# Performance work log

Measured on AMD Instinct MI355X. Metric: run time of the kernel, lower is better.

Reference implementation:

```python
import jax, jax.numpy as jnp
import numpy as np

D_MODEL = 1024
D_FF = 4096
N_EXPERTS = 8
TOP_K = 2
AUX_COEF = 0.01
ZLOSS_COEF = 0.001
EPS = 1e-9


def setup_inputs() -> dict:
    key = jax.random.key(0)
    k0, k1, k2, k3 = jax.random.split(key, 4)
    x = jax.random.normal(k0, (4, 2048, D_MODEL), dtype=jnp.float32)
    router_w = jax.random.normal(k1, (N_EXPERTS, D_MODEL), dtype=jnp.float32) * 0.02
    w1 = jax.random.normal(k2, (N_EXPERTS, D_FF, D_MODEL), dtype=jnp.float32) * 0.02
    b1 = jnp.zeros((N_EXPERTS, D_FF), dtype=jnp.float32)
    w2 = jax.random.normal(k3, (N_EXPERTS, D_MODEL, D_FF), dtype=jnp.float32) * 0.02
    b2 = jnp.zeros((N_EXPERTS, D_MODEL), dtype=jnp.float32)
    return {"x": x, "router_w": router_w, "w1": w1, "b1": b1, "w2": w2, "b2": b2}


def reference(x, router_w, w1, b1, w2, b2):
    B, T, D = x.shape
    N = B * T
    xf = x.reshape(N, D)

    # Router: logits [N, E], softmax probs, top-k selection + renormalized weights
    logits = jnp.einsum('nd,ed->ne', xf, router_w)
    probs = jax.nn.softmax(logits, axis=-1)
    topk_vals, topk_idx = jax.lax.top_k(probs, TOP_K)  # [N, K]
    topk_w = topk_vals / (topk_vals.sum(axis=-1, keepdims=True) + EPS)

    # Dense combine weights [N, E] (top-k indices are unique per row)
    combine = jnp.zeros((N, N_EXPERTS), dtype=xf.dtype)
    combine = combine.at[jnp.arange(N)[:, None], topk_idx].add(topk_w)

    # Per-expert MLP (fixed small loop over experts), weighted combine.
    # drop_tokens=False => no capacity truncation; masked-dense == gather/scatter math.
    y = jnp.zeros_like(xf)
    for e in range(N_EXPERTS):
        h = jax.nn.gelu(jnp.einsum('nd,fd->nf', xf, w1[e]) + b1[e], approximate=False)
        out_e = jnp.einsum('nf,df->nd', h, w2[e]) + b2[e]
        y = y + out_e * combine[:, e:e + 1]

    # Aux losses / stats
    importance = probs.sum(axis=0)                                   # [E]
    expert_load = jnp.zeros((N_EXPERTS,), jnp.float32).at[topk_idx.reshape(-1)].add(1.0)
    imp_n = importance / (importance.sum() + EPS)
    load_n = expert_load / (expert_load.sum() + EPS)
    balance_loss = N_EXPERTS * jnp.sum(imp_n * load_n)
    z_loss = jnp.mean(jax.nn.logsumexp(logits, axis=-1) ** 2)
    aux_loss = AUX_COEF * balance_loss + ZLOSS_COEF * z_loss

    return y.reshape(B, T, D), aux_loss, expert_load, importance
```

## Files before the change

### kernel.cpp

```cpp
#include <hip/hip_runtime.h>
#include <math.h>

#define NTOK 8192
#define DMODEL 1024
#define DFF 4096
#define NEXP 8
#define TILE 128
#define MAXTILES 136
#define MAXROWS (MAXTILES * TILE)
#define MOE_EPS 1e-9f
#define REG 4096

typedef unsigned short u16;
typedef __bf16 bf16x8 __attribute__((ext_vector_type(8)));
typedef float f32x4 __attribute__((ext_vector_type(4)));

struct Ctrl {
    int counts[NEXP];
    int fill[NEXP];
    int padded_off[NEXP];
    int n_tiles;
    int tile_expert[MAXTILES];
    int tile_base[MAXTILES];
    int tile_valid[MAXTILES];
    float imp[NEXP];
    float zacc;
};

__device__ __forceinline__ u16 f2bf(float f) {
    unsigned u = __float_as_uint(f);
    unsigned r = u + 0x7fffu + ((u >> 16) & 1u);
    return (u16)(r >> 16);
}

__device__ __forceinline__ void load16(const void* g, void* l) {
    __builtin_amdgcn_global_load_lds((__attribute__((address_space(1))) void*)g,
                                     (__attribute__((address_space(3))) void*)l,
                                     16, 0, 0);
}

__device__ __forceinline__ float gelu_fast(float h) {
    float u = h * (1.5957691216f + 0.0713548162f * h * h);
    return h / (1.f + __expf(-u));
}

__global__ __launch_bounds__(256) void k_convert(const float* __restrict__ src,
                                                 u16* __restrict__ dst, int n4) {
    int i = blockIdx.x * 256 + threadIdx.x;
    int stride = gridDim.x * 256;
    for (; i < n4; i += stride) {
        float4 v = ((const float4*)src)[i];
        ushort4 o;
        o.x = f2bf(v.x); o.y = f2bf(v.y); o.z = f2bf(v.z); o.w = f2bf(v.w);
        ((ushort4*)dst)[i] = o;
    }
}

__global__ __launch_bounds__(256) void k_router(const float* __restrict__ x,
                                                const float* __restrict__ rw,
                                                u16* __restrict__ xb,
                                                int* __restrict__ top_idx,
                                                float* __restrict__ top_w,
                                                Ctrl* __restrict__ ctrl) {
    __shared__ float srw[NEXP * DMODEL];
    __shared__ float simp[NEXP];
    __shared__ float szl;
    int tid = threadIdx.x;
    for (int i = tid; i < NEXP * DMODEL / 4; i += 256)
        ((float4*)srw)[i] = ((const float4*)rw)[i];
    if (tid < NEXP) simp[tid] = 0.f;
    if (tid == 0) szl = 0.f;
    __syncthreads();

    int lane = tid & 63;
    int n = blockIdx.x * 4 + (tid >> 6);
    float p[NEXP];
#pragma unroll
    for (int e = 0; e < NEXP; ++e) p[e] = 0.f;
    const float4* xr = (const float4*)(x + (size_t)n * DMODEL);
    u16 xs[16];
#pragma unroll
    for (int j = 0; j < 4; ++j) {
        float4 xv = xr[lane * 4 + j];
        int d = (lane * 4 + j) * 4;
        xs[j * 4 + 0] = f2bf(xv.x);
        xs[j * 4 + 1] = f2bf(xv.y);
        xs[j * 4 + 2] = f2bf(xv.z);
        xs[j * 4 + 3] = f2bf(xv.w);
#pragma unroll
        for (int e = 0; e < NEXP; ++e) {
            const float* r = srw + e * DMODEL + d;
            p[e] += xv.x * r[0] + xv.y * r[1] + xv.z * r[2] + xv.w * r[3];
        }
    }
    {
        uint4* dst = (uint4*)(xb + (size_t)n * DMODEL + lane * 16);
        dst[0] = ((const uint4*)xs)[0];
        dst[1] = ((const uint4*)xs)[1];
    }
#pragma unroll
    for (int e = 0; e < NEXP; ++e) {
#pragma unroll
        for (int off = 32; off > 0; off >>= 1) p[e] += __shfl_xor(p[e], off);
    }
    if (lane == 0) {
        float m = p[0];
#pragma unroll
        for (int e = 1; e < NEXP; ++e) m = fmaxf(m, p[e]);
        float pr[NEXP];
        float s = 0.f;
#pragma unroll
        for (int e = 0; e < NEXP; ++e) { pr[e] = expf(p[e] - m); s += pr[e]; }
        float inv = 1.f / s;
#pragma unroll
        for (int e = 0; e < NEXP; ++e) pr[e] *= inv;
        float lse = m + logf(s);
        int i0 = 0; float v0 = pr[0];
#pragma unroll
        for (int e = 1; e < NEXP; ++e) if (pr[e] > v0) { v0 = pr[e]; i0 = e; }
        int i1 = -1; float v1 = -1.f;
#pragma unroll
        for (int e = 0; e < NEXP; ++e) if (e != i0 && pr[e] > v1) { v1 = pr[e]; i1 = e; }
        float den = v0 + v1 + MOE_EPS;
        top_idx[n * 2] = i0;
        top_idx[n * 2 + 1] = i1;
        top_w[n * 2] = v0 / den;
        top_w[n * 2 + 1] = v1 / den;
#pragma unroll
        for (int e = 0; e < NEXP; ++e) atomicAdd(&simp[e], pr[e]);
        atomicAdd(&szl, lse * lse);
    }
    __syncthreads();
    if (tid < NEXP) atomicAdd(&ctrl->imp[tid], simp[tid]);
    if (tid == 255) atomicAdd(&ctrl->zacc, szl);
}

__global__ __launch_bounds__(256) void k_build(const int* __restrict__ top_idx,
                                               Ctrl* __restrict__ ctrl,
                                               int* __restrict__ tok_idx,
                                               float* __restrict__ tok_w) {
    __shared__ int cnt[NEXP];
    __shared__ int off[NEXP];
    __shared__ int tiles[NEXP];
    int tid = threadIdx.x;
    if (tid < NEXP) cnt[tid] = 0;
    __syncthreads();
    for (int i = tid; i < NTOK * 2; i += 256) atomicAdd(&cnt[top_idx[i]], 1);
    __syncthreads();
    if (tid == 0) {
        int o = 0, t = 0;
        for (int e = 0; e < NEXP; ++e) {
            int c = cnt[e];
            int te = (c + TILE - 1) / TILE;
            ctrl->counts[e] = c;
            ctrl->padded_off[e] = o;
            off[e] = o;
            tiles[e] = te;
            for (int i = 0; i < te; ++i) {
                ctrl->tile_expert[t] = e;
                ctrl->tile_base[t] = o + i * TILE;
                int v = c - i * TILE;
                ctrl->tile_valid[t] = v > TILE ? TILE : v;
                ++t;
            }
            o += te * TILE;
        }
        ctrl->n_tiles = t;
    }
    __syncthreads();
    for (int e = 0; e < NEXP; ++e) {
        int start = off[e] + cnt[e];
        int end = off[e] + tiles[e] * TILE;
        for (int i = start + tid; i < end; i += 256) {
            tok_idx[i] = 0;
            tok_w[i] = 0.f;
        }
    }
}

__global__ __launch_bounds__(256) void k_fill(const int* __restrict__ top_idx,
                                              const float* __restrict__ top_w,
                                              Ctrl* __restrict__ ctrl,
                                              int* __restrict__ tok_idx,
                                              float* __restrict__ tok_w) {
    int n = blockIdx.x * 256 + threadIdx.x;
    if (n >= NTOK) return;
#pragma unroll
    for (int k = 0; k < 2; ++k) {
        int e = top_idx[n * 2 + k];
        int pos = atomicAdd(&ctrl->fill[e], 1);
        int slot = ctrl->padded_off[e] + pos;
        tok_idx[slot] = n;
        tok_w[slot] = top_w[n * 2 + k];
    }
}

#define KLOOP3(STA, STB, NK)                                                          \
    STA(0, 0); STB(0, 0);                                                             \
    STA(1, 1); STB(1, 1);                                                             \
    for (int kt = 0; kt < (NK); ++kt) {                                               \
        int p = kt & 1;                                                               \
        if (kt < (NK) - 1) asm volatile("s_waitcnt vmcnt(4)" ::: "memory");           \
        else               asm volatile("s_waitcnt vmcnt(0)" ::: "memory");           \
        __builtin_amdgcn_s_barrier();                                                 \
        const u16* Ar = sA + p * REG;                                                 \
        const u16* Br = sB + p * REG;                                                 \
        bf16x8 a[4], b[4];                                                            \
        _Pragma("unroll") for (int m = 0; m < 4; ++m) a[m] = *(const bf16x8*)(Ar + aoff[m]); \
        _Pragma("unroll") for (int n = 0; n < 4; ++n) b[n] = *(const bf16x8*)(Br + boff[n]); \
        __builtin_amdgcn_s_setprio(1);                                                \
        _Pragma("unroll") for (int m = 0; m < 4; ++m)                                 \
            _Pragma("unroll") for (int n = 0; n < 4; ++n)                             \
                acc[m][n] = __builtin_amdgcn_mfma_f32_16x16x32_bf16(a[m], b[n], acc[m][n], 0, 0, 0); \
        __builtin_amdgcn_s_setprio(0);                                                \
        __builtin_amdgcn_s_barrier();                                                 \
        if (kt + 2 < (NK)) { STA(p, kt + 2); STB(p, kt + 2); }                        \
    }

__global__ __launch_bounds__(256, 4) void k_gemm1(const u16* __restrict__ xb,
                                                  const u16* __restrict__ w1b,
                                                  const float* __restrict__ b1,
                                                  const int* __restrict__ tok_idx,
                                                  const Ctrl* __restrict__ ctrl,
                                                  u16* __restrict__ H) {
    int flat = blockIdx.x;
    int t = (flat & 7) + ((flat >> 8) << 3);
    int n0 = ((flat >> 3) & 31) * TILE;
    if (t >= ctrl->n_tiles) return;
    int e = ctrl->tile_expert[t];
    int rbase = ctrl->tile_base[t];

    __shared__ __align__(16) u16 sA[2 * REG];
    __shared__ __align__(16) u16 sB[2 * REG];

    int tid = threadIdx.x;
    const u16* aS[2];
    const u16* bS[2];
    int fo[2];
#pragma unroll
    for (int q = 0; q < 2; ++q) {
        int f = q * 256 + tid;
        int row = f >> 2;
        int lc = (f & 3) ^ ((row >> 1) & 3);
        aS[q] = xb + (size_t)tok_idx[rbase + row] * DMODEL + lc * 8;
        bS[q] = w1b + (size_t)e * DFF * DMODEL + (size_t)(n0 + row) * DMODEL + lc * 8;
        fo[q] = f * 8;
    }

#define STA1(pp, kt)                                                                  \
    do { _Pragma("unroll") for (int q = 0; q < 2; ++q)                                \
        load16(aS[q] + (kt) * 32, &sA[(pp) * REG + fo[q]]); } while (0)
#define STB1(pp, kt)                                                                  \
    do { _Pragma("unroll") for (int q = 0; q < 2; ++q)                                \
        load16(bS[q] + (kt) * 32, &sB[(pp) * REG + fo[q]]); } while (0)

    int lane = tid & 63, w = tid >> 6;
    int wr = w >> 1, wc = w & 1;
    int l15 = lane & 15, lg = lane >> 4;
    int csw = (lg ^ ((l15 >> 1) & 3)) * 8;

    int aoff[4], boff[4];
#pragma unroll
    for (int m = 0; m < 4; ++m) aoff[m] = (wr * 64 + m * 16 + l15) * 32 + csw;
#pragma unroll
    for (int n = 0; n < 4; ++n) boff[n] = (wc * 64 + n * 16 + l15) * 32 + csw;

    f32x4 acc[4][4];
#pragma unroll
    for (int m = 0; m < 4; ++m)
#pragma unroll
        for (int n = 0; n < 4; ++n) acc[m][n] = (f32x4){0.f, 0.f, 0.f, 0.f};

    KLOOP3(STA1, STB1, DMODEL / 32)
#undef STA1
#undef STB1

    float bias[4];
#pragma unroll
    for (int n = 0; n < 4; ++n) bias[n] = b1[e * DFF + n0 + wc * 64 + n * 16 + l15];
#pragma unroll
    for (int m = 0; m < 4; ++m)
#pragma unroll
        for (int n = 0; n < 4; ++n) {
            int gcol = n0 + wc * 64 + n * 16 + l15;
#pragma unroll
            for (int r = 0; r < 4; ++r) {
                int grow = wr * 64 + m * 16 + lg * 4 + r;
                float h = acc[m][n][r] + bias[n];
                H[(size_t)(rbase + grow) * DFF + gcol] = f2bf(gelu_fast(h));
            }
        }
}

__global__ __launch_bounds__(256, 4) void k_gemm2(const u16* __restrict__ H,
                                                  const u16* __restrict__ w2b,
                                                  const float* __restrict__ b2,
                                                  const int* __restrict__ tok_idx,
                                                  const float* __restrict__ tok_w,
                                                  const Ctrl* __restrict__ ctrl,
                                                  float* __restrict__ y) {
    int flat = blockIdx.x;
    int t = (flat & 7) + ((flat >> 6) << 3);
    int n0 = ((flat >> 3) & 7) * TILE;
    if (t >= ctrl->n_tiles) return;
    int e = ctrl->tile_expert[t];
    int rbase = ctrl->tile_base[t];
    int valid = ctrl->tile_valid[t];

    __shared__ __align__(16) u16 sA[2 * REG];
    __shared__ __align__(16) u16 sB[2 * REG];

    int tid = threadIdx.x;
    const u16* aS[2];
    const u16* bS[2];
    int fo[2];
#pragma unroll
    for (int q = 0; q < 2; ++q) {
        int f = q * 256 + tid;
        int row = f >> 2;
        int lc = (f & 3) ^ ((row >> 1) & 3);
        aS[q] = H + (size_t)(rbase + row) * DFF + lc * 8;
        bS[q] = w2b + (size_t)e * DMODEL * DFF + (size_t)(n0 + row) * DFF + lc * 8;
        fo[q] = f * 8;
    }

#define STA2(pp, kt)                                                                  \
    do { _Pragma("unroll") for (int q = 0; q < 2; ++q)                                \
        load16(aS[q] + (kt) * 32, &sA[(pp) * REG + fo[q]]); } while (0)
#define STB2(pp, kt)                                                                  \
    do { _Pragma("unroll") for (int q = 0; q < 2; ++q)                                \
        load16(bS[q] + (kt) * 32, &sB[(pp) * REG + fo[q]]); } while (0)

    int lane = tid & 63, w = tid >> 6;
    int wr = w >> 1, wc = w & 1;
    int l15 = lane & 15, lg = lane >> 4;
    int csw = (lg ^ ((l15 >> 1) & 3)) * 8;

    int aoff[4], boff[4];
#pragma unroll
    for (int m = 0; m < 4; ++m) aoff[m] = (wr * 64 + m * 16 + l15) * 32 + csw;
#pragma unroll
    for (int n = 0; n < 4; ++n) boff[n] = (wc * 64 + n * 16 + l15) * 32 + csw;

    f32x4 acc[4][4];
#pragma unroll
    for (int m = 0; m < 4; ++m)
#pragma unroll
        for (int n = 0; n < 4; ++n) acc[m][n] = (f32x4){0.f, 0.f, 0.f, 0.f};

    KLOOP3(STA2, STB2, DFF / 32)
#undef STA2
#undef STB2

    float bias[4];
#pragma unroll
    for (int n = 0; n < 4; ++n) bias[n] = b2[e * DMODEL + n0 + wc * 64 + n * 16 + l15];
#pragma unroll
    for (int m = 0; m < 4; ++m)
#pragma unroll
        for (int n = 0; n < 4; ++n) {
            int gcol = n0 + wc * 64 + n * 16 + l15;
#pragma unroll
            for (int r = 0; r < 4; ++r) {
                int grow = wr * 64 + m * 16 + lg * 4 + r;
                if (grow < valid) {
                    int slot = rbase + grow;
                    int tok = tok_idx[slot];
                    float wgt = tok_w[slot];
                    unsafeAtomicAdd(&y[(size_t)tok * DMODEL + gcol],
                                    wgt * (acc[m][n][r] + bias[n]));
                }
            }
        }
}

__global__ void k_final(const Ctrl* __restrict__ ctrl, float* __restrict__ out) {
    if (blockIdx.x == 0 && threadIdx.x == 0) {
        float imp[NEXP], ld[NEXP];
        float imps = 0.f, loads = 0.f;
        for (int e = 0; e < NEXP; ++e) {
            imp[e] = ctrl->imp[e];
            ld[e] = (float)ctrl->counts[e];
            imps += imp[e];
            loads += ld[e];
        }
        float bal = 0.f;
        for (int e = 0; e < NEXP; ++e)
            bal += (imp[e] / (imps + MOE_EPS)) * (ld[e] / (loads + MOE_EPS));
        bal *= (float)NEXP;
        float z = ctrl->zacc / (float)NTOK;
        float aux = 0.01f * bal + 0.001f * z;
        size_t base = (size_t)NTOK * DMODEL;
        out[base] = aux;
        for (int e = 0; e < NEXP; ++e) out[base + 1 + e] = ld[e];
        for (int e = 0; e < NEXP; ++e) out[base + 9 + e] = imp[e];
    }
}

extern "C" void kernel_launch(void* const* d_in, const int* in_sizes, int n_in,
                              void* d_out, int out_size, void* d_ws, size_t ws_size,
                              hipStream_t stream) {
    (void)in_sizes; (void)n_in; (void)out_size; (void)ws_size;
    const float* x  = (const float*)d_in[0];
    const float* rw = (const float*)d_in[1];
    const float* w1 = (const float*)d_in[2];
    const float* b1 = (const float*)d_in[3];
    const float* w2 = (const float*)d_in[4];
    const float* b2 = (const float*)d_in[5];
    float* out = (float*)d_out;

    char* p = (char*)d_ws;
    Ctrl* ctrl = (Ctrl*)p;          p += 4096;
    u16* xb    = (u16*)p;           p += (size_t)NTOK * DMODEL * 2;
    u16* w1b   = (u16*)p;           p += (size_t)NEXP * DFF * DMODEL * 2;
    u16* w2b   = (u16*)p;           p += (size_t)NEXP * DMODEL * DFF * 2;
    u16* Hbuf  = (u16*)p;           p += (size_t)MAXROWS * DFF * 2;
    int* tok_idx = (int*)p;         p += (size_t)MAXROWS * 4;
    float* tok_w = (float*)p;       p += (size_t)MAXROWS * 4;
    int* tIdx  = (int*)p;           p += (size_t)NTOK * 2 * 4;
    float* tW  = (float*)p;         p += (size_t)NTOK * 2 * 4;

    hipMemsetAsync(ctrl, 0, sizeof(Ctrl), stream);
    hipMemsetAsync(d_out, 0, (size_t)NTOK * DMODEL * sizeof(float), stream);

    k_convert<<<2048, 256, 0, stream>>>(w1, w1b, NEXP * DFF * DMODEL / 4);
    k_convert<<<2048, 256, 0, stream>>>(w2, w2b, NEXP * DMODEL * DFF / 4);

    k_router<<<NTOK / 4, 256, 0, stream>>>(x, rw, xb, tIdx, tW, ctrl);
    k_build<<<1, 256, 0, stream>>>(tIdx, ctrl, tok_idx, tok_w);
    k_fill<<<NTOK / 256, 256, 0, stream>>>(tIdx, tW, ctrl, tok_idx, tok_w);

    k_gemm1<<<MAXTILES * (DFF / TILE), 256, 0, stream>>>(xb, w1b, b1, tok_idx, ctrl, Hbuf);
    k_gemm2<<<MAXTILES * (DMODEL / TILE), 256, 0, stream>>>(Hbuf, w2b, b2, tok_idx, tok_w, ctrl, out);

    k_final<<<1, 64, 0, stream>>>(ctrl, out);
}
```

Before: 750.5 us.

## Widen GEMM tiles to 128x256 with 512-thread blocks and 8 waves

Both expert GEMM kernels move from 128x128 output tiles with 4 waves to 128x256 tiles with 8 waves (a 2x4 wave grid). Each block now loads one A chunk per thread and a doubled B tile, so each A row fetched from shared memory is reused across twice as many output columns and the grid shrinks by half. The change raises shared memory per block to 48KB and puts 512 threads in a block, which may lower the number of resident blocks per CU and increase per-barrier synchronisation cost.

```diff
diff --git a/kernel.cpp b/kernel.cpp
--- a/kernel.cpp
+++ b/kernel.cpp
@@ -6,10 +6,12 @@
 #define DFF 4096
 #define NEXP 8
 #define TILE 128
+#define BN 256
 #define MAXTILES 136
 #define MAXROWS (MAXTILES * TILE)
 #define MOE_EPS 1e-9f
-#define REG 4096
+#define REGA 4096
+#define REGB 8192
 
 typedef unsigned short u16;
 typedef __bf16 bf16x8 __attribute__((ext_vector_type(8)));
@@ -195,16 +197,16 @@
     }
 }
 
-#define KLOOP3(STA, STB, NK)                                                          \
+#define KLOOP4(STA, STB, NK)                                                          \
     STA(0, 0); STB(0, 0);                                                             \
     STA(1, 1); STB(1, 1);                                                             \
     for (int kt = 0; kt < (NK); ++kt) {                                               \
         int p = kt & 1;                                                               \
-        if (kt < (NK) - 1) asm volatile("s_waitcnt vmcnt(4)" ::: "memory");           \
+        if (kt < (NK) - 1) asm volatile("s_waitcnt vmcnt(3)" ::: "memory");           \
         else               asm volatile("s_waitcnt vmcnt(0)" ::: "memory");           \
         __builtin_amdgcn_s_barrier();                                                 \
-        const u16* Ar = sA + p * REG;                                                 \
-        const u16* Br = sB + p * REG;                                                 \
+        const u16* Ar = sA + p * REGA;                                                \
+        const u16* Br = sB + p * REGB;                                                \
         bf16x8 a[4], b[4];                                                            \
         _Pragma("unroll") for (int m = 0; m < 4; ++m) a[m] = *(const bf16x8*)(Ar + aoff[m]); \
         _Pragma("unroll") for (int n = 0; n < 4; ++n) b[n] = *(const bf16x8*)(Br + boff[n]); \
@@ -217,45 +219,49 @@
         if (kt + 2 < (NK)) { STA(p, kt + 2); STB(p, kt + 2); }                        \
     }
 
-__global__ __launch_bounds__(256, 4) void k_gemm1(const u16* __restrict__ xb,
+__global__ __launch_bounds__(512, 4) void k_gemm1(const u16* __restrict__ xb,
                                                   const u16* __restrict__ w1b,
                                                   const float* __restrict__ b1,
                                                   const int* __restrict__ tok_idx,
                                                   const Ctrl* __restrict__ ctrl,
                                                   u16* __restrict__ H) {
     int flat = blockIdx.x;
-    int t = (flat & 7) + ((flat >> 8) << 3);
-    int n0 = ((flat >> 3) & 31) * TILE;
+    int t = (flat & 7) + ((flat >> 7) << 3);
+    int n0 = ((flat >> 3) & 15) * BN;
     if (t >= ctrl->n_tiles) return;
     int e = ctrl->tile_expert[t];
     int rbase = ctrl->tile_base[t];
 
-    __shared__ __align__(16) u16 sA[2 * REG];
-    __shared__ __align__(16) u16 sB[2 * REG];
+    __shared__ __align__(16) u16 sA[2 * REGA];
+    __shared__ __align__(16) u16 sB[2 * REGB];
 
     int tid = threadIdx.x;
-    const u16* aS[2];
+    const u16* aS;
+    int foA;
+    {
+        int row = tid >> 2;
+        int lc = (tid & 3) ^ ((row >> 1) & 3);
+        aS = xb + (size_t)tok_idx[rbase + row] * DMODEL + lc * 8;
+        foA = tid * 8;
+    }
     const u16* bS[2];
-    int fo[2];
+    int foB[2];
 #pragma unroll
     for (int q = 0; q < 2; ++q) {
-        int f = q * 256 + tid;
+        int f = q * 512 + tid;
         int row = f >> 2;
         int lc = (f & 3) ^ ((row >> 1) & 3);
-        aS[q] = xb + (size_t)tok_idx[rbase + row] * DMODEL + lc * 8;
         bS[q] = w1b + (size_t)e * DFF * DMODEL + (size_t)(n0 + row) * DMODEL + lc * 8;
-        fo[q] = f * 8;
-    }
-
-#define STA1(pp, kt)                                                                  \
-    do { _Pragma("unroll") for (int q = 0; q < 2; ++q)                                \
-        load16(aS[q] + (kt) * 32, &sA[(pp) * REG + fo[q]]); } while (0)
+        foB[q] = f * 8;
+    }
+
+#define STA1(pp, kt) do { load16(aS + (kt) * 32, &sA[(pp) * REGA + foA]); } while (0)
 #define STB1(pp, kt)                                                                  \
     do { _Pragma("unroll") for (int q = 0; q < 2; ++q)                                \
-        load16(bS[q] + (kt) * 32, &sB[(pp) * REG + fo[q]]); } while (0)
+        load16(bS[q] + (kt) * 32, &sB[(pp) * REGB + foB[q]]); } while (0)
 
     int lane = tid & 63, w = tid >> 6;
-    int wr = w >> 1, wc = w & 1;
+    int wr = w >> 2, wc = w & 3;
     int l15 = lane & 15, lg = lane >> 4;
     int csw = (lg ^ ((l15 >> 1) & 3)) * 8;
 
@@ -271,7 +277,7 @@
 #pragma unroll
         for (int n = 0; n < 4; ++n) acc[m][n] = (f32x4){0.f, 0.f, 0.f, 0.f};
 
-    KLOOP3(STA1, STB1, DMODEL / 32)
+    KLOOP4(STA1, STB1, DMODEL / 32)
 #undef STA1
 #undef STB1
 
@@ -292,7 +298,7 @@
         }
 }
 
-__global__ __launch_bounds__(256, 4) void k_gemm2(const u16* __restrict__ H,
+__global__ __launch_bounds__(512, 4) void k_gemm2(const u16* __restrict__ H,
                                                   const u16* __restrict__ w2b,
                                                   const float* __restrict__ b2,
                                                   const int* __restrict__ tok_idx,
@@ -300,39 +306,43 @@
                                                   const Ctrl* __restrict__ ctrl,
                                                   float* __restrict__ y) {
     int flat = blockIdx.x;
-    int t = (flat & 7) + ((flat >> 6) << 3);
-    int n0 = ((flat >> 3) & 7) * TILE;
+    int t = (flat & 7) + ((flat >> 5) << 3);
+    int n0 = ((flat >> 3) & 3) * BN;
     if (t >= ctrl->n_tiles) return;
     int e = ctrl->tile_expert[t];
     int rbase = ctrl->tile_base[t];
     int valid = ctrl->tile_valid[t];
 
-    __shared__ __align__(16) u16 sA[2 * REG];
-    __shared__ __align__(16) u16 sB[2 * REG];
+    __shared__ __align__(16) u16 sA[2 * REGA];
+    __shared__ __align__(16) u16 sB[2 * REGB];
 
     int tid = threadIdx.x;
-    const u16* aS[2];
+    const u16* aS;
+    int foA;
+    {
+        int row = tid >> 2;
+        int lc = (tid & 3) ^ ((row >> 1) & 3);
+        aS = H + (size_t)(rbase + row) * DFF + lc * 8;
+        foA = tid * 8;
+    }
     const u16* bS[2];
-    int fo[2];
+    int foB[2];
 #pragma unroll
     for (int q = 0; q < 2; ++q) {
-        int f = q * 256 + tid;
+        int f = q * 512 + tid;
         int row = f >> 2;
         int lc = (f & 3) ^ ((row >> 1) & 3);
-        aS[q] = H + (size_t)(rbase + row) * DFF + lc * 8;
         bS[q] = w2b + (size_t)e * DMODEL * DFF + (size_t)(n0 + row) * DFF + lc * 8;
-        fo[q] = f * 8;
-    }
-
-#define STA2(pp, kt)                                                                  \
-    do { _Pragma("unroll") for (int q = 0; q < 2; ++q)                                \
-        load16(aS[q] + (kt) * 32, &sA[(pp) * REG + fo[q]]); } while (0)
+        foB[q] = f * 8;
+    }
+
+#define STA2(pp, kt) do { load16(aS + (kt) * 32, &sA[(pp) * REGA + foA]); } while (0)
 #define STB2(pp, kt)                                                                  \
     do { _Pragma("unroll") for (int q = 0; q < 2; ++q)                                \
-        load16(bS[q] + (kt) * 32, &sB[(pp) * REG + fo[q]]); } while (0)
+        load16(bS[q] + (kt) * 32, &sB[(pp) * REGB + foB[q]]); } while (0)
 
     int lane = tid & 63, w = tid >> 6;
-    int wr = w >> 1, wc = w & 1;
+    int wr = w >> 2, wc = w & 3;
     int l15 = lane & 15, lg = lane >> 4;
     int csw = (lg ^ ((l15 >> 1) & 3)) * 8;
 
@@ -348,7 +358,7 @@
 #pragma unroll
         for (int n = 0; n < 4; ++n) acc[m][n] = (f32x4){0.f, 0.f, 0.f, 0.f};
 
-    KLOOP3(STA2, STB2, DFF / 32)
+    KLOOP4(STA2, STB2, DFF / 32)
 #undef STA2
 #undef STB2
 
@@ -430,8 +440,8 @@
     k_build<<<1, 256, 0, stream>>>(tIdx, ctrl, tok_idx, tok_w);
     k_fill<<<NTOK / 256, 256, 0, stream>>>(tIdx, tW, ctrl, tok_idx, tok_w);
 
-    k_gemm1<<<MAXTILES * (DFF / TILE), 256, 0, stream>>>(xb, w1b, b1, tok_idx, ctrl, Hbuf);
-    k_gemm2<<<MAXTILES * (DMODEL / TILE), 256, 0, stream>>>(Hbuf, w2b, b2, tok_idx, tok_w, ctrl, out);
+    k_gemm1<<<MAXTILES * (DFF / BN), 512, 0, stream>>>(xb, w1b, b1, tok_idx, ctrl, Hbuf);
+    k_gemm2<<<MAXTILES * (DMODEL / BN), 512, 0, stream>>>(Hbuf, w2b, b2, tok_idx, tok_w, ctrl, out);
 
     k_final<<<1, 64, 0, stream>>>(ctrl, out);
 }
```

Result: slower. 773.1 us (+3.0%).
